# Kernel tuning notes

Hardware: AMD Instinct MI355X
Metric: run time of the kernel (lower is better)

## Reference

```python
import jax, jax.numpy as jnp
import numpy as np

BIT_WIDTH = 8
APOT_M = 2
APOT_K = BIT_WIDTH // APOT_M  # 4


def _build_codebook() -> np.ndarray:
    # base levels: 0 plus powers 2^0 .. 2^-(2^k - 2)
    base = np.array([0.0] + [2.0 ** (-i) for i in range(2 ** APOT_K - 1)], dtype=np.float64)
    sums = base
    for _ in range(APOT_M - 1):
        sums = (sums[:, None] + base[None, :]).ravel()
    levels = np.unique(sums)
    levels = levels / levels.max()
    pos = levels[levels > 0.0]
    cb = np.sort(np.concatenate([-pos, np.array([0.0]), pos]))
    return cb.astype(np.float32)  # K = 243 for (8, 2)


def setup_inputs() -> dict:
    key = jax.random.key(0)
    x = jax.random.normal(key, (4096, 8192), dtype=jnp.float32)
    # alpha would be initialized to max|x| on the first call; use a typical value.
    alpha = jnp.asarray(2.5, dtype=jnp.float32)
    codebook = jnp.asarray(_build_codebook())
    return {"x": x, "alpha": alpha, "codebook": codebook}


def reference(x, alpha, codebook):
    # eval-mode forward (weight_norm stats path only active in training)
    alpha_pos = jnp.abs(alpha) + 1e-5
    x_norm = jnp.clip(x / alpha_pos, -1.0, 1.0)
    # nearest codebook entry via binary search on the sorted codebook —
    # identical to argmin(|x - cb|) with torch's first-index tie-break.
    K = codebook.shape[0]
    i = jnp.clip(jnp.searchsorted(codebook, x_norm), 1, K - 1)
    left = codebook[i - 1]
    right = codebook[i]
    # tie -> smaller index (left), matching torch.argmin
    x_q_norm = jnp.where(jnp.abs(x_norm - left) <= jnp.abs(x_norm - right), left, right)
    # straight-through estimator
    x_q_norm = jax.lax.stop_gradient(x_q_norm - x_norm) + x_norm
    return x_q_norm * alpha_pos
```

## Files before the change

kernel.cpp:

```cpp
#include <hip/hip_runtime.h>


typedef float vfloat4 __attribute__((ext_vector_type(4)));

__device__ __forceinline__ float apot_q(float xn) {
    const unsigned u = __float_as_uint(xn);
    const unsigned s = u & 0x80000000u;
    const unsigned a = u & 0x7FFFFFFFu;
    unsigned q;
    if (a >= 0x38000000u) {
        const unsigned e    = a >> 23;
        const unsigned m    = a & 0x7FFFFFu;
        const unsigned base = a - m;
        const unsigned g    = 1u << (135u - e);
        const unsigned L    = 31u - __clz(m | 1u);
        const unsigned bit  = 1u << L;
        const bool fine = (m < g);
        const unsigned lo  = fine ? base       : (base | bit);
        const unsigned hi  = fine ? (base + g) : (base + (bit << 1));
        const unsigned mid = fine ? g : (bit + (bit << 1));
        const unsigned m2  = m + m;
        const bool pickLo = (m2 < mid) | ((m2 == mid) & (s == 0u));
        q = pickLo ? lo : hi;
    } else {
        const unsigned T0 = 0x37800000u;
        const bool pickZero = (a < T0) | ((a == T0) & (s == 0u));
        q = pickZero ? 0u : 0x38000000u;
    }
    return __uint_as_float(q | s);
}

__device__ __forceinline__ vfloat4 quant4(vfloat4 v, float alpha_pos) {
    vfloat4 o;
    #pragma unroll
    for (int e = 0; e < 4; ++e) {
        float xn = fminf(1.0f, fmaxf(-1.0f, v[e] / alpha_pos));
        o[e] = apot_q(xn) * alpha_pos;
    }
    return o;
}

__global__ __launch_bounds__(256) void apot_quant_kernel(
    const float* __restrict__ x,
    const float* __restrict__ alpha,
    float* __restrict__ out,
    int n)
{
    const float alpha_pos = fabsf(alpha[0]) + 1e-5f;

    const int blockStart = blockIdx.x * (256 * 8);
    const int i0 = blockStart + (int)threadIdx.x * 4;
    const int i1 = i0 + 256 * 4;

    if (i1 + 3 < n) {
        vfloat4 v0 = __builtin_nontemporal_load((const vfloat4*)(x + i0));
        vfloat4 v1 = __builtin_nontemporal_load((const vfloat4*)(x + i1));
        vfloat4 o0 = quant4(v0, alpha_pos);
        vfloat4 o1 = quant4(v1, alpha_pos);
        __builtin_nontemporal_store(o0, (vfloat4*)(out + i0));
        __builtin_nontemporal_store(o1, (vfloat4*)(out + i1));
    } else {
        for (int k = 0; k < 8; ++k) {
            int idx = blockStart + (int)threadIdx.x * 4;
            idx = (k < 4) ? (idx + k) : (idx + 1024 + (k - 4));
            if (idx < n) {
                float xn = fminf(1.0f, fmaxf(-1.0f, x[idx] / alpha_pos));
                out[idx] = apot_q(xn) * alpha_pos;
            }
        }
    }
}

extern "C" void kernel_launch(void* const* d_in, const int* in_sizes, int n_in,
                              void* d_out, int out_size, void* d_ws, size_t ws_size,
                              hipStream_t stream) {
    const float* x     = (const float*)d_in[0];
    const float* alpha = (const float*)d_in[1];
    float* out         = (float*)d_out;

    const int n = in_sizes[0];
    const int elemsPerBlock = 256 * 8;
    const int grid = (n + elemsPerBlock - 1) / elemsPerBlock;

    apot_quant_kernel<<<grid, 256, 0, stream>>>(x, alpha, out, n);
}
```

Before: 222.6 us.

## Use grid-stride loop with software-prefetched float4 loads and fixed grid

Replaces the one-shot block-per-2048-elements launch with a persistent grid of at most 2048 blocks. Each thread walks the array with a grid stride and loads the next float4 before quantizing the current one. Loads switch from nontemporal to regular. The aim is to cut block launch overhead and hide memory latency through prefetching, at the cost of fewer bytes in flight per thread per iteration. The tail handling also assumes n is a multiple of 4 for every thread except the last.

```diff
diff --git a/kernel.cpp b/kernel.cpp
--- a/kernel.cpp
+++ b/kernel.cpp
@@ -48,27 +48,29 @@
 {
     const float alpha_pos = fabsf(alpha[0]) + 1e-5f;
 
-    const int blockStart = blockIdx.x * (256 * 8);
-    const int i0 = blockStart + (int)threadIdx.x * 4;
-    const int i1 = i0 + 256 * 4;
+    const int stride4 = (int)(gridDim.x * blockDim.x) * 4;
+    int idx = (int)(blockIdx.x * blockDim.x + threadIdx.x) * 4;
 
-    if (i1 + 3 < n) {
-        vfloat4 v0 = __builtin_nontemporal_load((const vfloat4*)(x + i0));
-        vfloat4 v1 = __builtin_nontemporal_load((const vfloat4*)(x + i1));
-        vfloat4 o0 = quant4(v0, alpha_pos);
-        vfloat4 o1 = quant4(v1, alpha_pos);
-        __builtin_nontemporal_store(o0, (vfloat4*)(out + i0));
-        __builtin_nontemporal_store(o1, (vfloat4*)(out + i1));
-    } else {
-        for (int k = 0; k < 8; ++k) {
-            int idx = blockStart + (int)threadIdx.x * 4;
-            idx = (k < 4) ? (idx + k) : (idx + 1024 + (k - 4));
-            if (idx < n) {
-                float xn = fminf(1.0f, fmaxf(-1.0f, x[idx] / alpha_pos));
-                out[idx] = apot_q(xn) * alpha_pos;
-            }
+    if (idx + 3 >= n) {
+        for (int k = idx; k < n; ++k) {
+            float xn = fminf(1.0f, fmaxf(-1.0f, x[k] / alpha_pos));
+            out[k] = apot_q(xn) * alpha_pos;
         }
+        return;
     }
+
+    const int iters = (n - idx - 4) / stride4 + 1;
+
+    vfloat4 cur = *(const vfloat4*)(x + idx);
+    #pragma unroll 2
+    for (int k = 1; k < iters; ++k) {
+        const vfloat4 nxt = *(const vfloat4*)(x + idx + stride4);
+        const vfloat4 o = quant4(cur, alpha_pos);
+        __builtin_nontemporal_store(o, (vfloat4*)(out + idx));
+        cur = nxt;
+        idx += stride4;
+    }
+    __builtin_nontemporal_store(quant4(cur, alpha_pos), (vfloat4*)(out + idx));
 }
 
 extern "C" void kernel_launch(void* const* d_in, const int* in_sizes, int n_in,
@@ -79,8 +81,10 @@
     float* out         = (float*)d_out;
 
     const int n = in_sizes[0];
-    const int elemsPerBlock = 256 * 8;
-    const int grid = (n + elemsPerBlock - 1) / elemsPerBlock;
+    const int block = 256;
+    int grid = 2048;
+    const int maxTiles = (n + block * 4 - 1) / (block * 4);
+    if (grid > maxTiles) grid = maxTiles;
 
-    apot_quant_kernel<<<grid, 256, 0, stream>>>(x, alpha, out, n);
+    apot_quant_kernel<<<grid, block, 0, stream>>>(x, alpha, out, n);
 }
```

Result: slower. 238.2 us (+7.0%).
